# Kernel optimization log

Hardware: AMD Instinct MI355X
Metric: run time of the kernel (lower is better)

Reference implementation:

```python
import jax, jax.numpy as jnp
import numpy as np

B, C, T, H, NCLS = 512, 22, 1000, 64, 4


def setup_inputs() -> dict:
    key = jax.random.key(0)
    ks = jax.random.split(key, 8)
    s_ih = 1.0 / np.sqrt(H)
    x = jax.random.normal(ks[0], (B, C, T), dtype=jnp.float32)
    # PyTorch LSTM params: gate order [i, f, g, o], each of size H
    W_ih = jax.random.uniform(ks[1], (4 * H, C), minval=-s_ih, maxval=s_ih, dtype=jnp.float32)
    W_hh = jax.random.uniform(ks[2], (4 * H, H), minval=-s_ih, maxval=s_ih, dtype=jnp.float32)
    b_ih = jax.random.uniform(ks[3], (4 * H,), minval=-s_ih, maxval=s_ih, dtype=jnp.float32)
    b_hh = jax.random.uniform(ks[4], (4 * H,), minval=-s_ih, maxval=s_ih, dtype=jnp.float32)
    s_fc = 1.0 / np.sqrt(H * T)
    W_fc = jax.random.uniform(ks[5], (NCLS, H * T), minval=-s_fc, maxval=s_fc, dtype=jnp.float32)
    b_fc = jax.random.uniform(ks[6], (NCLS,), minval=-s_fc, maxval=s_fc, dtype=jnp.float32)
    return {"x": x, "W_ih": W_ih, "W_hh": W_hh, "b_ih": b_ih, "b_hh": b_hh,
            "W_fc": W_fc, "b_fc": b_fc}


def _lstm(xs, W_ih, W_hh, b_ih, b_hh):
    # xs: [B, T, C] -> outputs [B, T, H]
    b = xs.shape[0]
    # precompute input projections for all timesteps: [T, B, 4H]
    x_proj = jnp.einsum('btc,gc->tbg', xs, W_ih) + (b_ih + b_hh)
    h0 = jnp.zeros((b, W_hh.shape[1]), xs.dtype)
    c0 = jnp.zeros_like(h0)

    def step(carry, xp):
        h, c = carry
        gates = xp + h @ W_hh.T  # [B, 4H]
        i, f, g, o = jnp.split(gates, 4, axis=-1)
        i = jax.nn.sigmoid(i)
        f = jax.nn.sigmoid(f)
        g = jnp.tanh(g)
        o = jax.nn.sigmoid(o)
        c = f * c + i * g
        h = o * jnp.tanh(c)
        return (h, c), h

    _, hs = jax.lax.scan(step, (h0, c0), x_proj)  # hs: [T, B, H]
    return jnp.transpose(hs, (1, 0, 2))  # [B, T, H]


def reference(x, W_ih, W_hh, b_ih, b_hh, W_fc, b_fc):
    xs = jnp.transpose(x, (0, 2, 1))  # [B, T, C]  (permute(0,2,1))
    hs = _lstm(xs, W_ih, W_hh, b_ih, b_hh)  # [B, T, H]
    flat = hs.reshape(hs.shape[0], -1)  # [B, T*H], time-major per row
    logits = flat @ W_fc.T + b_fc  # [B, 4]
    return jax.nn.softmax(logits, axis=1)
```

## Files before the change

### kernel.cpp

```cpp
#include <hip/hip_runtime.h>

#define BB   512
#define CC   22
#define TT   1000
#define HH   64
#define NCLS 4
#define TC   250
#define NCHUNK (TT / TC)
#define XROW 12

typedef _Float16 f16;
typedef __attribute__((ext_vector_type(2))) _Float16 h2;

__device__ __forceinline__ float sigm(float x) {
    return 1.0f / (1.0f + __expf(-x));
}
__device__ __forceinline__ float tanh_(float x) {
    float e = __expf(-2.0f * fabsf(x));
    float r = (1.0f - e) / (1.0f + e);
    return copysignf(r, x);
}

__global__ __launch_bounds__(64, 1) void lstm_wave(
    const float* __restrict__ x,
    const float* __restrict__ W_ih,
    const float* __restrict__ W_hh,
    const float* __restrict__ b_ih,
    const float* __restrict__ b_hh,
    const float* __restrict__ W_fc,
    const float* __restrict__ b_fc,
    float* __restrict__ out)
{
    __shared__ __align__(16) h2  xs[TC][XROW];
    __shared__ __align__(16) f16 hbuf[HH];

    const int lane = threadIdx.x;
    const int r    = blockIdx.x;

    h2 whh[4][32];
    h2 wih[4][11];
    float bias[4];
    #pragma unroll
    for (int g = 0; g < 4; ++g) {
        const int row = g * HH + lane;
        const float* wr = W_hh + row * HH;
        #pragma unroll
        for (int k = 0; k < 32; ++k)
            whh[g][k] = h2{(f16)wr[2 * k], (f16)wr[2 * k + 1]};
        const float* wi = W_ih + row * CC;
        #pragma unroll
        for (int k = 0; k < 11; ++k)
            wih[g][k] = h2{(f16)wi[2 * k], (f16)wi[2 * k + 1]};
        bias[g] = b_ih[row] + b_hh[row];
    }

    hbuf[lane] = (f16)0.0f;
    float c = 0.0f;
    float fc0 = 0.f, fc1 = 0.f, fc2 = 0.f, fc3 = 0.f;
    const float* p0 = W_fc + 0 * (TT * HH) + lane;
    const float* p1 = W_fc + 1 * (TT * HH) + lane;
    const float* p2 = W_fc + 2 * (TT * HH) + lane;
    const float* p3 = W_fc + 3 * (TT * HH) + lane;
    const float* xrow = x + (size_t)r * (CC * TT);

    for (int chunk = 0; chunk < NCHUNK; ++chunk) {
        for (int tb = 0; tb < TC; tb += 64) {
            const int t = tb + lane;
            if (t < TC) {
                const float* gx = xrow + chunk * TC + t;
                union { h2 h[XROW]; uint4 q[3]; } U;
                #pragma unroll
                for (int k = 0; k < 11; ++k)
                    U.h[k] = h2{(f16)gx[(2 * k) * TT], (f16)gx[(2 * k + 1) * TT]};
                U.h[11] = h2{(f16)0.0f, (f16)0.0f};
                uint4* dst = (uint4*)&xs[t][0];
                dst[0] = U.q[0]; dst[1] = U.q[1]; dst[2] = U.q[2];
            }
        }

        for (int tt = 0; tt < TC; ++tt) {
            union { uint4 q[8]; h2 h[32]; } H;
            const uint4* hr = (const uint4*)hbuf;
            #pragma unroll
            for (int i = 0; i < 8; ++i) H.q[i] = hr[i];

            union { uint4 q[3]; h2 h[XROW]; } X;
            const uint4* xr = (const uint4*)&xs[tt][0];
            X.q[0] = xr[0]; X.q[1] = xr[1]; X.q[2] = xr[2];

            float w0 = *p0, w1 = *p1, w2 = *p2, w3 = *p3;
            p0 += HH; p1 += HH; p2 += HH; p3 += HH;

            float a0 = bias[0], a1 = bias[1], a2 = bias[2], a3 = bias[3];
            #pragma unroll
            for (int k = 0; k < 11; ++k) {
                a0 = __builtin_amdgcn_fdot2(X.h[k], wih[0][k], a0, false);
                a1 = __builtin_amdgcn_fdot2(X.h[k], wih[1][k], a1, false);
                a2 = __builtin_amdgcn_fdot2(X.h[k], wih[2][k], a2, false);
                a3 = __builtin_amdgcn_fdot2(X.h[k], wih[3][k], a3, false);
            }
            #pragma unroll
            for (int k = 0; k < 32; ++k) {
                a0 = __builtin_amdgcn_fdot2(H.h[k], whh[0][k], a0, false);
                a1 = __builtin_amdgcn_fdot2(H.h[k], whh[1][k], a1, false);
                a2 = __builtin_amdgcn_fdot2(H.h[k], whh[2][k], a2, false);
                a3 = __builtin_amdgcn_fdot2(H.h[k], whh[3][k], a3, false);
            }

            float iv = sigm(a0), fv = sigm(a1), gv = tanh_(a2), ov = sigm(a3);
            c = fv * c + iv * gv;
            float h = ov * tanh_(c);

            fc0 += h * w0; fc1 += h * w1; fc2 += h * w2; fc3 += h * w3;

            hbuf[lane] = (f16)h;
        }
    }

    #pragma unroll
    for (int off = 32; off; off >>= 1) {
        fc0 += __shfl_down(fc0, off);
        fc1 += __shfl_down(fc1, off);
        fc2 += __shfl_down(fc2, off);
        fc3 += __shfl_down(fc3, off);
    }
    if (lane == 0) {
        float l0 = fc0 + b_fc[0], l1 = fc1 + b_fc[1];
        float l2 = fc2 + b_fc[2], l3 = fc3 + b_fc[3];
        float m  = fmaxf(fmaxf(l0, l1), fmaxf(l2, l3));
        float e0 = __expf(l0 - m), e1 = __expf(l1 - m);
        float e2 = __expf(l2 - m), e3 = __expf(l3 - m);
        float s  = e0 + e1 + e2 + e3;
        float4 o; o.x = e0 / s; o.y = e1 / s; o.z = e2 / s; o.w = e3 / s;
        *(float4*)(out + r * NCLS) = o;
    }
}

extern "C" void kernel_launch(void* const* d_in, const int* in_sizes, int n_in,
                              void* d_out, int out_size, void* d_ws, size_t ws_size,
                              hipStream_t stream) {
    const float* x    = (const float*)d_in[0];
    const float* W_ih = (const float*)d_in[1];
    const float* W_hh = (const float*)d_in[2];
    const float* b_ih = (const float*)d_in[3];
    const float* b_hh = (const float*)d_in[4];
    const float* W_fc = (const float*)d_in[5];
    const float* b_fc = (const float*)d_in[6];
    float* out = (float*)d_out;

    lstm_wave<<<BB, 64, 0, stream>>>(x, W_ih, W_hh, b_ih, b_hh, W_fc, b_fc, out);
}
```

Baseline: 683.6 us.

## Split LSTM gate dot products across four waves with an LDS reduction

New measurement: 1.011 ms. 47.9% more time.

```diff
diff --git a/kernel.cpp b/kernel.cpp
--- a/kernel.cpp
+++ b/kernel.cpp
@@ -7,10 +7,11 @@
 #define NCLS 4
 #define TC   250
 #define NCHUNK (TT / TC)
-#define XROW 12
 
 typedef _Float16 f16;
 typedef __attribute__((ext_vector_type(2))) _Float16 h2;
+
+union PU { unsigned u; h2 h; };
 
 __device__ __forceinline__ float sigm(float x) {
     return 1.0f / (1.0f + __expf(-x));
@@ -21,7 +22,7 @@
     return copysignf(r, x);
 }
 
-__global__ __launch_bounds__(64, 1) void lstm_wave(
+__global__ __launch_bounds__(256, 2) void lstm_splitk(
     const float* __restrict__ x,
     const float* __restrict__ W_ih,
     const float* __restrict__ W_hh,
@@ -31,108 +32,148 @@
     const float* __restrict__ b_fc,
     float* __restrict__ out)
 {
-    __shared__ __align__(16) h2  xs[TC][XROW];
-    __shared__ __align__(16) f16 hbuf[HH];
+    __shared__ __align__(16) unsigned xs[TC * 16];
+    __shared__ __align__(16) f16 hb[4][HH];
+    __shared__ float pbf[2][NCLS][4][HH];
 
-    const int lane = threadIdx.x;
+    const int tid  = threadIdx.x;
+    const int w    = tid >> 6;
+    const int lane = tid & 63;
     const int r    = blockIdx.x;
 
-    h2 whh[4][32];
-    h2 wih[4][11];
-    float bias[4];
+    unsigned wgt[4][12];
+    float bias0 = 0.f, bias1 = 0.f, bias2 = 0.f, bias3 = 0.f;
     #pragma unroll
     for (int g = 0; g < 4; ++g) {
         const int row = g * HH + lane;
-        const float* wr = W_hh + row * HH;
         #pragma unroll
-        for (int k = 0; k < 32; ++k)
-            whh[g][k] = h2{(f16)wr[2 * k], (f16)wr[2 * k + 1]};
-        const float* wi = W_ih + row * CC;
-        #pragma unroll
-        for (int k = 0; k < 11; ++k)
-            wih[g][k] = h2{(f16)wi[2 * k], (f16)wi[2 * k + 1]};
-        bias[g] = b_ih[row] + b_hh[row];
+        for (int i = 0; i < 12; ++i) {
+            const int s = 12 * w + i;
+            float lo, hi;
+            if (s < 32) {
+                lo = W_hh[row * HH + 2 * s];
+                hi = W_hh[row * HH + 2 * s + 1];
+            } else {
+                const int c0 = 2 * (s - 32);
+                lo = (c0     < CC) ? W_ih[row * CC + c0]     : 0.f;
+                hi = (c0 + 1 < CC) ? W_ih[row * CC + c0 + 1] : 0.f;
+            }
+            PU pu; pu.h = h2{(f16)lo, (f16)hi};
+            wgt[g][i] = pu.u;
+        }
+    }
+    if (w == 0) {
+        bias0 = b_ih[0 * HH + lane] + b_hh[0 * HH + lane];
+        bias1 = b_ih[1 * HH + lane] + b_hh[1 * HH + lane];
+        bias2 = b_ih[2 * HH + lane] + b_hh[2 * HH + lane];
+        bias3 = b_ih[3 * HH + lane] + b_hh[3 * HH + lane];
     }
 
-    hbuf[lane] = (f16)0.0f;
+    hb[w][lane] = (f16)0.0f;
     float c = 0.0f;
     float fc0 = 0.f, fc1 = 0.f, fc2 = 0.f, fc3 = 0.f;
-    const float* p0 = W_fc + 0 * (TT * HH) + lane;
-    const float* p1 = W_fc + 1 * (TT * HH) + lane;
-    const float* p2 = W_fc + 2 * (TT * HH) + lane;
-    const float* p3 = W_fc + 3 * (TT * HH) + lane;
     const float* xrow = x + (size_t)r * (CC * TT);
+    int p = 0;
 
     for (int chunk = 0; chunk < NCHUNK; ++chunk) {
-        for (int tb = 0; tb < TC; tb += 64) {
-            const int t = tb + lane;
-            if (t < TC) {
-                const float* gx = xrow + chunk * TC + t;
-                union { h2 h[XROW]; uint4 q[3]; } U;
-                #pragma unroll
-                for (int k = 0; k < 11; ++k)
-                    U.h[k] = h2{(f16)gx[(2 * k) * TT], (f16)gx[(2 * k + 1) * TT]};
-                U.h[11] = h2{(f16)0.0f, (f16)0.0f};
-                uint4* dst = (uint4*)&xs[t][0];
-                dst[0] = U.q[0]; dst[1] = U.q[1]; dst[2] = U.q[2];
+        for (int t = tid; t < TC; t += 256) {
+            const float* gx = xrow + chunk * TC + t;
+            unsigned q[16];
+            #pragma unroll
+            for (int k = 0; k < 16; ++k) {
+                const int c0 = 2 * k, c1 = 2 * k + 1;
+                float lo = (c0 < CC) ? gx[c0 * TT] : 0.f;
+                float hi = (c1 < CC) ? gx[c1 * TT] : 0.f;
+                PU pu; pu.h = h2{(f16)lo, (f16)hi};
+                q[k] = pu.u;
             }
+            uint4* dst = (uint4*)&xs[t * 16];
+            dst[0] = *(uint4*)&q[0];  dst[1] = *(uint4*)&q[4];
+            dst[2] = *(uint4*)&q[8];  dst[3] = *(uint4*)&q[12];
         }
+        __syncthreads();
 
         for (int tt = 0; tt < TC; ++tt) {
-            union { uint4 q[8]; h2 h[32]; } H;
-            const uint4* hr = (const uint4*)hbuf;
+            const int t = chunk * TC + tt;
+
+            union { uint4 q[3]; unsigned u[12]; } Bv;
+            const uint4* hq = (const uint4*)&hb[w][0];
+            const uint4* xq = (const uint4*)&xs[tt * 16];
+            if      (w == 0) { Bv.q[0] = hq[0]; Bv.q[1] = hq[1]; Bv.q[2] = hq[2]; }
+            else if (w == 1) { Bv.q[0] = hq[3]; Bv.q[1] = hq[4]; Bv.q[2] = hq[5]; }
+            else if (w == 2) { Bv.q[0] = hq[6]; Bv.q[1] = hq[7]; Bv.q[2] = xq[0]; }
+            else             { Bv.q[0] = xq[1]; Bv.q[1] = xq[2]; Bv.q[2] = xq[3]; }
+
+            float wv0 = 0.f, wv1 = 0.f, wv2 = 0.f, wv3 = 0.f;
+            if (w == 0) {
+                const float* pf = W_fc + t * HH + lane;
+                wv0 = pf[0];
+                wv1 = pf[TT * HH];
+                wv2 = pf[2 * TT * HH];
+                wv3 = pf[3 * TT * HH];
+            }
+
+            float a0 = bias0, a1 = bias1, a2 = bias2, a3 = bias3;
             #pragma unroll
-            for (int i = 0; i < 8; ++i) H.q[i] = hr[i];
+            for (int i = 0; i < 12; ++i) {
+                PU b;  b.u  = Bv.u[i];
+                PU g0; g0.u = wgt[0][i];
+                PU g1; g1.u = wgt[1][i];
+                PU g2; g2.u = wgt[2][i];
+                PU g3; g3.u = wgt[3][i];
+                a0 = __builtin_amdgcn_fdot2(b.h, g0.h, a0, false);
+                a1 = __builtin_amdgcn_fdot2(b.h, g1.h, a1, false);
+                a2 = __builtin_amdgcn_fdot2(b.h, g2.h, a2, false);
+                a3 = __builtin_amdgcn_fdot2(b.h, g3.h, a3, false);
+            }
 
-            union { uint4 q[3]; h2 h[XROW]; } X;
-            const uint4* xr = (const uint4*)&xs[tt][0];
-            X.q[0] = xr[0]; X.q[1] = xr[1]; X.q[2] = xr[2];
+            pbf[p][0][w][lane] = a0;
+            pbf[p][1][w][lane] = a1;
+            pbf[p][2][w][lane] = a2;
+            pbf[p][3][w][lane] = a3;
+            __syncthreads();
 
-            float w0 = *p0, w1 = *p1, w2 = *p2, w3 = *p3;
-            p0 += HH; p1 += HH; p2 += HH; p3 += HH;
-
-            float a0 = bias[0], a1 = bias[1], a2 = bias[2], a3 = bias[3];
-            #pragma unroll
-            for (int k = 0; k < 11; ++k) {
-                a0 = __builtin_amdgcn_fdot2(X.h[k], wih[0][k], a0, false);
-                a1 = __builtin_amdgcn_fdot2(X.h[k], wih[1][k], a1, false);
-                a2 = __builtin_amdgcn_fdot2(X.h[k], wih[2][k], a2, false);
-                a3 = __builtin_amdgcn_fdot2(X.h[k], wih[3][k], a3, false);
-            }
-            #pragma unroll
-            for (int k = 0; k < 32; ++k) {
-                a0 = __builtin_amdgcn_fdot2(H.h[k], whh[0][k], a0, false);
-                a1 = __builtin_amdgcn_fdot2(H.h[k], whh[1][k], a1, false);
-                a2 = __builtin_amdgcn_fdot2(H.h[k], whh[2][k], a2, false);
-                a3 = __builtin_amdgcn_fdot2(H.h[k], whh[3][k], a3, false);
-            }
+            const int wa = (w + 1) & 3, wb = (w + 2) & 3, wc = (w + 3) & 3;
+            float r00 = pbf[p][0][wa][lane], r01 = pbf[p][0][wb][lane], r02 = pbf[p][0][wc][lane];
+            float r10 = pbf[p][1][wa][lane], r11 = pbf[p][1][wb][lane], r12 = pbf[p][1][wc][lane];
+            float r20 = pbf[p][2][wa][lane], r21 = pbf[p][2][wb][lane], r22 = pbf[p][2][wc][lane];
+            float r30 = pbf[p][3][wa][lane], r31 = pbf[p][3][wb][lane], r32 = pbf[p][3][wc][lane];
+            a0 += (r00 + r01) + r02;
+            a1 += (r10 + r11) + r12;
+            a2 += (r20 + r21) + r22;
+            a3 += (r30 + r31) + r32;
 
             float iv = sigm(a0), fv = sigm(a1), gv = tanh_(a2), ov = sigm(a3);
             c = fv * c + iv * gv;
             float h = ov * tanh_(c);
 
-            fc0 += h * w0; fc1 += h * w1; fc2 += h * w2; fc3 += h * w3;
+            if (w == 0) {
+                fc0 += h * wv0; fc1 += h * wv1; fc2 += h * wv2; fc3 += h * wv3;
+            }
 
-            hbuf[lane] = (f16)h;
+            hb[w][lane] = (f16)h;
+            p ^= 1;
         }
     }
 
-    #pragma unroll
-    for (int off = 32; off; off >>= 1) {
-        fc0 += __shfl_down(fc0, off);
-        fc1 += __shfl_down(fc1, off);
-        fc2 += __shfl_down(fc2, off);
-        fc3 += __shfl_down(fc3, off);
-    }
-    if (lane == 0) {
-        float l0 = fc0 + b_fc[0], l1 = fc1 + b_fc[1];
-        float l2 = fc2 + b_fc[2], l3 = fc3 + b_fc[3];
-        float m  = fmaxf(fmaxf(l0, l1), fmaxf(l2, l3));
-        float e0 = __expf(l0 - m), e1 = __expf(l1 - m);
-        float e2 = __expf(l2 - m), e3 = __expf(l3 - m);
-        float s  = e0 + e1 + e2 + e3;
-        float4 o; o.x = e0 / s; o.y = e1 / s; o.z = e2 / s; o.w = e3 / s;
-        *(float4*)(out + r * NCLS) = o;
+    if (w == 0) {
+        #pragma unroll
+        for (int off = 32; off; off >>= 1) {
+            fc0 += __shfl_down(fc0, off);
+            fc1 += __shfl_down(fc1, off);
+            fc2 += __shfl_down(fc2, off);
+            fc3 += __shfl_down(fc3, off);
+        }
+        if (lane == 0) {
+            float l0 = fc0 + b_fc[0], l1 = fc1 + b_fc[1];
+            float l2 = fc2 + b_fc[2], l3 = fc3 + b_fc[3];
+            float m  = fmaxf(fmaxf(l0, l1), fmaxf(l2, l3));
+            float e0 = __expf(l0 - m), e1 = __expf(l1 - m);
+            float e2 = __expf(l2 - m), e3 = __expf(l3 - m);
+            float s  = e0 + e1 + e2 + e3;
+            float4 o; o.x = e0 / s; o.y = e1 / s; o.z = e2 / s; o.w = e3 / s;
+            *(float4*)(out + r * NCLS) = o;
+        }
     }
 }
 
@@ -148,5 +189,5 @@
     const float* b_fc = (const float*)d_in[6];
     float* out = (float*)d_out;
 
-    lstm_wave<<<BB, 64, 0, stream>>>(x, W_ih, W_hh, b_ih, b_hh, W_fc, b_fc, out);
+    lstm_splitk<<<BB, 256, 0, stream>>>(x, W_ih, W_hh, b_ih, b_hh, W_fc, b_fc, out);
 }
```
